# Optimization experiments

Measured on AMD Instinct MI355X. Metric: run time of the kernel, lower is better.

The kernel has to match this reference:

```python
import jax, jax.numpy as jnp
import numpy as np

N_NODES = 100000
N_EDGES = 1600000
D_FEAT = 64
NUM_HEADS = 4
HEAD_CH = 16
ALPHA = 0.2  # leaky_relu negative slope (Keras default)


def setup_inputs() -> dict:
    key = jax.random.key(0)
    ks = jax.random.split(key, 8)
    hc = NUM_HEADS * HEAD_CH
    scale = 1.0 / np.sqrt(D_FEAT)
    return {
        'node_features': jax.random.normal(ks[0], (N_NODES, D_FEAT), jnp.float32),
        'Wq': jax.random.normal(ks[1], (D_FEAT, hc), jnp.float32) * scale,
        'bq': jnp.zeros((hc,), jnp.float32),
        'Wv': jax.random.normal(ks[2], (D_FEAT, hc), jnp.float32) * scale,
        'bv': jnp.zeros((hc,), jnp.float32),
        'attn_kernel': jax.random.normal(ks[3], (HEAD_CH, NUM_HEADS), jnp.float32) / np.sqrt(HEAD_CH),
        'edge_source': jax.random.randint(ks[4], (N_EDGES,), 0, N_NODES, jnp.int32),
        'edge_target': jax.random.randint(ks[5], (N_EDGES,), 0, N_NODES, jnp.int32),
    }


def _gatv2(node_features, Wq, bq, Wv, bv, attn_kernel, edge_source, edge_target):
    # Dense transforms on nodes (small GEMMs), then reshape to heads.
    query = (node_features @ Wq + bq).reshape(N_NODES, NUM_HEADS, HEAD_CH)
    value = (node_features @ Wv + bv).reshape(N_NODES, NUM_HEADS, HEAD_CH)
    # Gather onto edges: receiver query, sender value.
    q_e = query[edge_target]           # [E, H, C]
    v_e = value[edge_source]           # [E, H, C]
    feat = jax.nn.leaky_relu(q_e + v_e, ALPHA)
    # EinsumDense '...ik,ki->...i' with kernel [C, H]
    logits = jnp.einsum('ehc,ch->eh', feat, attn_kernel)  # [E, H]
    # Segment softmax over receiver neighborhoods.
    seg_max = jax.ops.segment_max(logits, edge_target, num_segments=N_NODES)
    seg_max = jnp.where(jnp.isfinite(seg_max), seg_max, 0.0)
    exp = jnp.exp(logits - seg_max[edge_target])           # [E, H]
    denom = jax.ops.segment_sum(exp, edge_target, num_segments=N_NODES)
    denom = jnp.where(denom > 0, denom, 1.0)
    coef = exp / denom[edge_target]                        # [E, H]
    # Weighted scatter-sum of values to receivers.
    pooled = jax.ops.segment_sum(coef[:, :, None] * v_e, edge_target,
                                 num_segments=N_NODES)     # [N, H, C]
    out = pooled.reshape(N_NODES, NUM_HEADS * HEAD_CH)
    # NOTE: source code sets final activation to attention_activation (leaky_relu).
    return jax.nn.leaky_relu(out, ALPHA)


def reference(node_features, Wq, bq, Wv, bv, attn_kernel, edge_source, edge_target):
    return _gatv2(node_features, Wq, bq, Wv, bv, attn_kernel, edge_source, edge_target)
```

## Files before the change

kernel.cpp:

```cpp
#include <hip/hip_runtime.h>

#define NN 100000
#define NE 1600000
#define ALPHA 0.2f

#define BSH   9
#define NPBK  512
#define NBUCK ((NN + NPBK - 1) / NPBK)
#define NPB   256
#define CHUNK ((NE + NPB - 1) / NPB)

#define MTILES (NN / 16)
#define TBLKS  ((MTILES + 3) / 4)

typedef __attribute__((ext_vector_type(8))) short  short8;
typedef __attribute__((ext_vector_type(4))) float  f32x4;

__device__ __forceinline__ unsigned short f2bf(float f) {
    unsigned int u = __builtin_bit_cast(unsigned int, f);
    u += 0x7FFFu + ((u >> 16) & 1u);
    return (unsigned short)(u >> 16);
}
__device__ __forceinline__ float bf2fs(unsigned short u) {
    return __builtin_bit_cast(float, (unsigned int)u << 16);
}
__device__ __forceinline__ float bflo(unsigned int u) {
    return __builtin_bit_cast(float, u << 16);
}
__device__ __forceinline__ float bfhi(unsigned int u) {
    return __builtin_bit_cast(float, u & 0xFFFF0000u);
}

template<int CTRL>
__device__ __forceinline__ float dpp_add(float x) {
    int y = __builtin_amdgcn_update_dpp(0, __builtin_bit_cast(int, x),
                                        CTRL, 0xF, 0xF, true);
    return x + __builtin_bit_cast(float, y);
}

__device__ __forceinline__ int block_excl_scan_256(int val, int* lds4) {
    const int lane = threadIdx.x & 63;
    const int wid  = threadIdx.x >> 6;
    int incl = val;
    #pragma unroll
    for (int off = 1; off < 64; off <<= 1) {
        int t = __shfl_up(incl, off);
        if (lane >= off) incl += t;
    }
    if (lane == 63) lds4[wid] = incl;
    __syncthreads();
    int wbase = 0;
    #pragma unroll
    for (int w = 0; w < 4; w++) if (w < wid) wbase += lds4[w];
    __syncthreads();
    return wbase + incl - val;
}

__device__ __forceinline__ int block_excl_scan_512(int val, int* lds8) {
    const int lane = threadIdx.x & 63;
    const int wid  = threadIdx.x >> 6;
    int incl = val;
    #pragma unroll
    for (int off = 1; off < 64; off <<= 1) {
        int t = __shfl_up(incl, off);
        if (lane >= off) incl += t;
    }
    if (lane == 63) lds8[wid] = incl;
    __syncthreads();
    int wbase = 0;
    #pragma unroll
    for (int w = 0; w < 8; w++) if (w < wid) wbase += lds8[w];
    __syncthreads();
    return wbase + incl - val;
}

__global__ __launch_bounds__(256) void fused_tc_kernel(
    const float* __restrict__ nf, const float* __restrict__ Wq, const float* __restrict__ bq,
    const float* __restrict__ Wv, const float* __restrict__ bv,
    unsigned short* __restrict__ qbf, unsigned short* __restrict__ vbf,
    const int* __restrict__ etgt, int* __restrict__ hist)
{
    __shared__ short8 sB[2][2][8][64];
    __shared__ float  sbias[128];
    __shared__ int    h[NBUCK];
    const int tid = threadIdx.x;

    if (blockIdx.x < NPB) {
        const int blk = blockIdx.x;
        for (int i = tid; i < NBUCK; i += 256) h[i] = 0;
        __syncthreads();
        const int e0 = blk * CHUNK;
        const int e1 = min(e0 + CHUNK, NE);
        for (int e = e0 + tid; e < e1; e += 256)
            atomicAdd(&h[etgt[e] >> BSH], 1);
        __syncthreads();
        for (int i = tid; i < NBUCK; i += 256)
            hist[blk * NBUCK + i] = h[i];
        return;
    }

    if (tid < 64)       sbias[tid] = bq[tid];
    else if (tid < 128) sbias[tid] = bv[tid - 64];

    for (int slot = tid; slot < 2 * 8 * 64; slot += 256) {
        const int lane  = slot & 63;
        const int ntile = (slot >> 6) & 7;
        const int kstep = slot >> 9;
        const int j     = ntile * 16 + (lane & 15);
        const int kbase = kstep * 32 + (lane >> 4) * 8;
        const float* W  = (j < 64) ? Wq : Wv;
        const int jj    = j & 63;
        short8 hi, lo;
        #pragma unroll
        for (int r = 0; r < 8; r++) {
            float w = W[(kbase + r) * 64 + jj];
            unsigned short hh = f2bf(w);
            lo[r] = (short)f2bf(w - bf2fs(hh));
            hi[r] = (short)hh;
        }
        sB[0][kstep][ntile][lane] = hi;
        sB[1][kstep][ntile][lane] = lo;
    }
    __syncthreads();

    const int lane  = tid & 63;
    const int wv_   = tid >> 6;
    const int row16 = lane & 15;
    const int kg    = lane >> 4;
    const int tb    = blockIdx.x - NPB;

    for (int wt = tb * 4 + wv_; wt < MTILES; wt += TBLKS * 4) {
        const int row = wt * 16 + row16;

        short8 ah[2];
        #pragma unroll
        for (int s = 0; s < 2; s++) {
            const float* ap = nf + (size_t)row * 64 + s * 32 + kg * 8;
            #pragma unroll
            for (int r = 0; r < 8; r++)
                ah[s][r] = (short)f2bf(ap[r]);
        }

        #pragma unroll
        for (int nt = 0; nt < 8; nt++) {
            f32x4 acc = {0.f, 0.f, 0.f, 0.f};
            #pragma unroll
            for (int s = 0; s < 2; s++) {
                acc = __builtin_amdgcn_mfma_f32_16x16x32_bf16(ah[s], sB[0][s][nt][lane], acc, 0, 0, 0);
                acc = __builtin_amdgcn_mfma_f32_16x16x32_bf16(ah[s], sB[1][s][nt][lane], acc, 0, 0, 0);
            }
            const int col = nt * 16 + (lane & 15);
            const float b = sbias[col];
            unsigned short* outp = (col < 64) ? qbf : vbf;
            const int jj    = col & 63;
            const int rbase = wt * 16 + (lane >> 4) * 4;
            #pragma unroll
            for (int r = 0; r < 4; r++)
                outp[(size_t)(rbase + r) * 64 + jj] = f2bf(acc[r] + b);
        }
    }
}

__global__ __launch_bounds__(256) void colbase_kernel(
    const int* __restrict__ hist,
    int* __restrict__ bbase, int* __restrict__ colbase, int* __restrict__ offs)
{
    __shared__ int lds4[4];
    __shared__ int sb[256];
    const int bk = blockIdx.x;
    const int t  = threadIdx.x;

    int csum = 0;
    if (t < NBUCK) {
        #pragma unroll 8
        for (int b = 0; b < NPB; b++) csum += hist[b * NBUCK + t];
    }
    int gex = block_excl_scan_256(csum, lds4);
    sb[t] = gex;
    if (t == bk) bbase[bk] = gex;
    if (bk == 0 && t == NBUCK - 1) { bbase[NBUCK] = gex + csum; offs[NN] = NE; }
    __syncthreads();
    const int myBase = sb[bk];
    __syncthreads();

    int val = hist[t * NBUCK + bk];
    int ex  = block_excl_scan_256(val, lds4);
    colbase[t * NBUCK + bk] = myBase + ex;
}

__global__ __launch_bounds__(256) void partition_kernel(
    const int* __restrict__ esrc, const int* __restrict__ etgt,
    const int* __restrict__ colbase, unsigned int* __restrict__ packed)
{
    __shared__ int cur[NBUCK];
    const int blk = blockIdx.x;
    for (int i = threadIdx.x; i < NBUCK; i += 256)
        cur[i] = colbase[blk * NBUCK + i];
    __syncthreads();
    const int e0 = blk * CHUNK;
    const int e1 = min(e0 + CHUNK, NE);
    for (int e = e0 + threadIdx.x; e < e1; e += 256) {
        int t = etgt[e], s = esrc[e];
        int bk = t >> BSH;
        int pos = atomicAdd(&cur[bk], 1);
        packed[pos] = (unsigned)s | ((unsigned)(t & (NPBK - 1)) << 17);
    }
}

__global__ __launch_bounds__(512) void bucket_csr_kernel(
    const unsigned int* __restrict__ packed, const int* __restrict__ bbase,
    int* __restrict__ offs, int* __restrict__ ssrc)
{
    __shared__ int cnt[NPBK];
    __shared__ int lds8[8];
    const int bk  = blockIdx.x;
    const int tid = threadIdx.x;
    const int s0 = bbase[bk], s1 = bbase[bk + 1];
    cnt[tid] = 0;
    __syncthreads();
    for (int e = s0 + tid; e < s1; e += 512)
        atomicAdd(&cnt[packed[e] >> 17], 1);
    __syncthreads();
    int a  = cnt[tid];
    int ex = block_excl_scan_512(a, lds8);
    const int node = (bk << BSH) + tid;
    const int g = s0 + ex;
    if (node < NN) offs[node] = g;
    __syncthreads();
    cnt[tid] = g;
    __syncthreads();
    for (int e = s0 + tid; e < s1; e += 512) {
        unsigned p = packed[e];
        int pos = atomicAdd(&cnt[p >> 17], 1);
        ssrc[pos] = (int)(p & 0x1FFFFu);
    }
}

__device__ __forceinline__ uint4 ldraw16(const unsigned short* __restrict__ vb,
                                         int src, int s8) {
    return *(const uint4*)((const char*)vb + ((size_t)src << 7) + s8 * 16);
}

__global__ __launch_bounds__(256) void gather_kernel(
    const unsigned short* __restrict__ qb, const unsigned short* __restrict__ vb,
    const float* __restrict__ ak,
    const int* __restrict__ offs, const int* __restrict__ ssrc,
    float* __restrict__ out)
{
    const int node = (blockIdx.x * 256 + threadIdx.x) >> 6;
    const int lane = threadIdx.x & 63;
    if (node >= NN) return;
    const int eslot = lane >> 3;
    const int s8    = lane & 7;
    const int h     = s8 >> 1;

    const int start = offs[node];
    const int end   = offs[node + 1];

    if (start >= end) {
        if (lane < 8) {
            float4 z{0.f, 0.f, 0.f, 0.f};
            *(float4*)(out + (size_t)node * 64 + s8 * 8)     = z;
            *(float4*)(out + (size_t)node * 64 + s8 * 8 + 4) = z;
        }
        return;
    }
    const int end1 = end - 1;

    const float c6 = 0.6f * 1.44269504088896f;
    const float c4 = 0.4f * 1.44269504088896f;
    float a6[8], a4[8];
    #pragma unroll
    for (int j = 0; j < 8; j++) {
        float k = ak[((s8 & 1) * 8 + j) * 4 + h];
        a6[j] = c6 * k;  a4[j] = c4 * k;
    }

    const uint4 qraw = *(const uint4*)((const char*)qb + ((size_t)node << 7) + s8 * 16);
    float q[8];
    q[0] = bflo(qraw.x); q[1] = bfhi(qraw.x);
    q[2] = bflo(qraw.y); q[3] = bfhi(qraw.y);
    q[4] = bflo(qraw.z); q[5] = bfhi(qraw.z);
    q[6] = bflo(qraw.w); q[7] = bfhi(qraw.w);

    int i0 = ssrc[min(start +     eslot, end1)];
    int i1 = ssrc[min(start + 8 + eslot, end1)];
    uint4 rr0 = ldraw16(vb, i0, s8);
    uint4 rr1 = ldraw16(vb, i1, s8);
    int mi0 = ssrc[min(start + 16 + eslot, end1)];
    int mi1 = ssrc[min(start + 24 + eslot, end1)];

    float acc[8] = {0.f, 0.f, 0.f, 0.f, 0.f, 0.f, 0.f, 0.f};
    float ws = 0.f;

    for (int p = start; p < end; p += 16) {
        {
            float v[8];
            v[0] = bflo(rr0.x); v[1] = bfhi(rr0.x);
            v[2] = bflo(rr0.y); v[3] = bfhi(rr0.y);
            v[4] = bflo(rr0.z); v[5] = bfhi(rr0.z);
            v[6] = bflo(rr0.w); v[7] = bfhi(rr0.w);
            rr0 = ldraw16(vb, mi0, s8);
            mi0 = ssrc[min(p + 32 + eslot, end1)];
            float x = 0.f;
            #pragma unroll
            for (int j = 0; j < 8; j++) {
                float f = q[j] + v[j];
                x = fmaf(f, a6[j], x);
                x = fmaf(fabsf(f), a4[j], x);
            }
            x = dpp_add<0xB1>(x);
            float w = (p + eslot < end) ? __builtin_amdgcn_exp2f(x) : 0.f;
            ws += w;
            #pragma unroll
            for (int j = 0; j < 8; j++) acc[j] = fmaf(w, v[j], acc[j]);
        }
        {
            float v[8];
            v[0] = bflo(rr1.x); v[1] = bfhi(rr1.x);
            v[2] = bflo(rr1.y); v[3] = bfhi(rr1.y);
            v[4] = bflo(rr1.z); v[5] = bfhi(rr1.z);
            v[6] = bflo(rr1.w); v[7] = bfhi(rr1.w);
            rr1 = ldraw16(vb, mi1, s8);
            mi1 = ssrc[min(p + 40 + eslot, end1)];
            float x = 0.f;
            #pragma unroll
            for (int j = 0; j < 8; j++) {
                float f = q[j] + v[j];
                x = fmaf(f, a6[j], x);
                x = fmaf(fabsf(f), a4[j], x);
            }
            x = dpp_add<0xB1>(x);
            float w = (p + 8 + eslot < end) ? __builtin_amdgcn_exp2f(x) : 0.f;
            ws += w;
            #pragma unroll
            for (int j = 0; j < 8; j++) acc[j] = fmaf(w, v[j], acc[j]);
        }
    }

    #pragma unroll
    for (int m = 8; m <= 32; m <<= 1) {
        #pragma unroll
        for (int j = 0; j < 8; j++) acc[j] += __shfl_xor(acc[j], m);
        ws += __shfl_xor(ws, m);
    }

    if (lane < 8) {
        float inv = (ws > 0.f) ? __frcp_rn(ws) : 1.0f;
        float r[8];
        #pragma unroll
        for (int j = 0; j < 8; j++) {
            float t = acc[j] * inv;
            r[j] = fmaxf(t, ALPHA * t);
        }
        *(float4*)(out + (size_t)node * 64 + s8 * 8)     = float4{r[0], r[1], r[2], r[3]};
        *(float4*)(out + (size_t)node * 64 + s8 * 8 + 4) = float4{r[4], r[5], r[6], r[7]};
    }
}

extern "C" void kernel_launch(void* const* d_in, const int* in_sizes, int n_in,
                              void* d_out, int out_size, void* d_ws, size_t ws_size,
                              hipStream_t stream) {
    const float* nf   = (const float*)d_in[0];
    const float* Wq   = (const float*)d_in[1];
    const float* bq   = (const float*)d_in[2];
    const float* Wv   = (const float*)d_in[3];
    const float* bv   = (const float*)d_in[4];
    const float* ak   = (const float*)d_in[5];
    const int*   esrc = (const int*)d_in[6];
    const int*   etgt = (const int*)d_in[7];
    float* out = (float*)d_out;

    unsigned short* qbf     = (unsigned short*)d_ws;
    unsigned short* vbf     = qbf + (size_t)NN * 64;
    int*            offs    = (int*)(vbf + (size_t)NN * 64);
    int*            ssrc    = offs + (NN + 1);
    unsigned int*   packed  = (unsigned int*)(ssrc + NE);
    int*            hist    = (int*)(packed + NE);
    int*            colbase = hist + NPB * NBUCK;
    int*            bbase   = colbase + NPB * NBUCK;

    fused_tc_kernel<<<NPB + TBLKS, 256, 0, stream>>>(nf, Wq, bq, Wv, bv, qbf, vbf,
                                                     etgt, hist);
    colbase_kernel<<<NBUCK, 256, 0, stream>>>(hist, bbase, colbase, offs);
    partition_kernel<<<NPB, 256, 0, stream>>>(esrc, etgt, colbase, packed);
    bucket_csr_kernel<<<NBUCK, 512, 0, stream>>>(packed, bbase, offs, ssrc);
    gather_kernel<<<(NN * 64 + 255) / 256, 256, 0, stream>>>(qbf, vbf, ak, offs, ssrc, out);
}
```

Before: 113.1 us.

## Spread node transform tiles across all CSR-build kernels to fill idle CUs

The dense Q/V transform is no longer done in one kernel alongside the histogram. Its tiles are split into four fixed ranges, and each range is appended as extra blocks to the histogram, colbase, partition and bucket-CSR kernels. The aim is to overlap the MFMA GEMM work with the latency-bound sort stages, which underuse the GPU. In exchange, every transform block repeats the weight split/prep into shared memory, and the hardcoded tile ranges must cover all tiles exactly.

```diff
diff --git a/kernel.cpp b/kernel.cpp
--- a/kernel.cpp
+++ b/kernel.cpp
@@ -11,7 +11,15 @@
 #define CHUNK ((NE + NPB - 1) / NPB)
 
 #define MTILES (NN / 16)
-#define TBLKS  ((MTILES + 3) / 4)
+
+#define TB1 0
+#define N1  290
+#define TB2 1160
+#define N2  145
+#define TB3 1740
+#define N3  638
+#define TB4 4292
+#define N4  245
 
 typedef __attribute__((ext_vector_type(8))) short  short8;
 typedef __attribute__((ext_vector_type(4))) float  f32x4;
@@ -74,35 +82,14 @@
     return wbase + incl - val;
 }
 
-__global__ __launch_bounds__(256) void fused_tc_kernel(
-    const float* __restrict__ nf, const float* __restrict__ Wq, const float* __restrict__ bq,
+__device__ __forceinline__ void transform_prep(
+    const float* __restrict__ Wq, const float* __restrict__ bq,
     const float* __restrict__ Wv, const float* __restrict__ bv,
-    unsigned short* __restrict__ qbf, unsigned short* __restrict__ vbf,
-    const int* __restrict__ etgt, int* __restrict__ hist)
-{
-    __shared__ short8 sB[2][2][8][64];
-    __shared__ float  sbias[128];
-    __shared__ int    h[NBUCK];
-    const int tid = threadIdx.x;
-
-    if (blockIdx.x < NPB) {
-        const int blk = blockIdx.x;
-        for (int i = tid; i < NBUCK; i += 256) h[i] = 0;
-        __syncthreads();
-        const int e0 = blk * CHUNK;
-        const int e1 = min(e0 + CHUNK, NE);
-        for (int e = e0 + tid; e < e1; e += 256)
-            atomicAdd(&h[etgt[e] >> BSH], 1);
-        __syncthreads();
-        for (int i = tid; i < NBUCK; i += 256)
-            hist[blk * NBUCK + i] = h[i];
-        return;
-    }
-
+    short8 (*sB)[2][8][64], float* sbias, int tid, int nthr)
+{
     if (tid < 64)       sbias[tid] = bq[tid];
     else if (tid < 128) sbias[tid] = bv[tid - 64];
-
-    for (int slot = tid; slot < 2 * 8 * 64; slot += 256) {
+    for (int slot = tid; slot < 2 * 8 * 64; slot += nthr) {
         const int lane  = slot & 63;
         const int ntile = (slot >> 6) & 7;
         const int kstep = slot >> 9;
@@ -121,119 +108,187 @@
         sB[0][kstep][ntile][lane] = hi;
         sB[1][kstep][ntile][lane] = lo;
     }
-    __syncthreads();
-
-    const int lane  = tid & 63;
-    const int wv_   = tid >> 6;
-    const int row16 = lane & 15;
-    const int kg    = lane >> 4;
-    const int tb    = blockIdx.x - NPB;
-
-    for (int wt = tb * 4 + wv_; wt < MTILES; wt += TBLKS * 4) {
-        const int row = wt * 16 + row16;
-
-        short8 ah[2];
+}
+
+__device__ __forceinline__ void transform_tile(
+    const float* __restrict__ nf,
+    unsigned short* __restrict__ qbf, unsigned short* __restrict__ vbf,
+    short8 (*sB)[2][8][64], const float* sbias, int wt, int lane)
+{
+    const int row = wt * 16 + (lane & 15);
+    short8 ah[2];
+    #pragma unroll
+    for (int s = 0; s < 2; s++) {
+        const float* ap = nf + (size_t)row * 64 + s * 32 + (lane >> 4) * 8;
+        #pragma unroll
+        for (int r = 0; r < 8; r++)
+            ah[s][r] = (short)f2bf(ap[r]);
+    }
+    #pragma unroll
+    for (int nt = 0; nt < 8; nt++) {
+        f32x4 acc = {0.f, 0.f, 0.f, 0.f};
         #pragma unroll
         for (int s = 0; s < 2; s++) {
-            const float* ap = nf + (size_t)row * 64 + s * 32 + kg * 8;
-            #pragma unroll
-            for (int r = 0; r < 8; r++)
-                ah[s][r] = (short)f2bf(ap[r]);
-        }
-
-        #pragma unroll
-        for (int nt = 0; nt < 8; nt++) {
-            f32x4 acc = {0.f, 0.f, 0.f, 0.f};
-            #pragma unroll
-            for (int s = 0; s < 2; s++) {
-                acc = __builtin_amdgcn_mfma_f32_16x16x32_bf16(ah[s], sB[0][s][nt][lane], acc, 0, 0, 0);
-                acc = __builtin_amdgcn_mfma_f32_16x16x32_bf16(ah[s], sB[1][s][nt][lane], acc, 0, 0, 0);
-            }
-            const int col = nt * 16 + (lane & 15);
-            const float b = sbias[col];
-            unsigned short* outp = (col < 64) ? qbf : vbf;
-            const int jj    = col & 63;
-            const int rbase = wt * 16 + (lane >> 4) * 4;
-            #pragma unroll
-            for (int r = 0; r < 4; r++)
-                outp[(size_t)(rbase + r) * 64 + jj] = f2bf(acc[r] + b);
-        }
-    }
-}
-
-__global__ __launch_bounds__(256) void colbase_kernel(
+            acc = __builtin_amdgcn_mfma_f32_16x16x32_bf16(ah[s], sB[0][s][nt][lane], acc, 0, 0, 0);
+            acc = __builtin_amdgcn_mfma_f32_16x16x32_bf16(ah[s], sB[1][s][nt][lane], acc, 0, 0, 0);
+        }
+        const int col = nt * 16 + (lane & 15);
+        const float b = sbias[col];
+        unsigned short* outp = (col < 64) ? qbf : vbf;
+        const int jj    = col & 63;
+        const int rbase = wt * 16 + (lane >> 4) * 4;
+        #pragma unroll
+        for (int r = 0; r < 4; r++)
+            outp[(size_t)(rbase + r) * 64 + jj] = f2bf(acc[r] + b);
+    }
+}
+
+__global__ __launch_bounds__(256) void k1_hist_tf(
+    const float* __restrict__ nf, const float* __restrict__ Wq, const float* __restrict__ bq,
+    const float* __restrict__ Wv, const float* __restrict__ bv,
+    unsigned short* __restrict__ qbf, unsigned short* __restrict__ vbf,
+    const int* __restrict__ etgt, int* __restrict__ hist)
+{
+    __shared__ short8 sB[2][2][8][64];
+    __shared__ float  sbias[128];
+    __shared__ int    h[NBUCK];
+    const int tid = threadIdx.x;
+
+    if (blockIdx.x < NPB) {
+        const int blk = blockIdx.x;
+        for (int i = tid; i < NBUCK; i += 256) h[i] = 0;
+        __syncthreads();
+        const int e0 = blk * CHUNK;
+        const int e1 = min(e0 + CHUNK, NE);
+        for (int e = e0 + tid; e < e1; e += 256)
+            atomicAdd(&h[etgt[e] >> BSH], 1);
+        __syncthreads();
+        for (int i = tid; i < NBUCK; i += 256)
+            hist[blk * NBUCK + i] = h[i];
+        return;
+    }
+
+    transform_prep(Wq, bq, Wv, bv, sB, sbias, tid, 256);
+    __syncthreads();
+    const int wt = TB1 + ((int)blockIdx.x - NPB) * 4 + (tid >> 6);
+    if (wt < MTILES) transform_tile(nf, qbf, vbf, sB, sbias, wt, tid & 63);
+}
+
+__global__ __launch_bounds__(256) void k2_colbase_tf(
+    const float* __restrict__ nf, const float* __restrict__ Wq, const float* __restrict__ bq,
+    const float* __restrict__ Wv, const float* __restrict__ bv,
+    unsigned short* __restrict__ qbf, unsigned short* __restrict__ vbf,
     const int* __restrict__ hist,
     int* __restrict__ bbase, int* __restrict__ colbase, int* __restrict__ offs)
 {
+    __shared__ short8 sB[2][2][8][64];
+    __shared__ float  sbias[128];
     __shared__ int lds4[4];
     __shared__ int sb[256];
-    const int bk = blockIdx.x;
-    const int t  = threadIdx.x;
-
-    int csum = 0;
-    if (t < NBUCK) {
-        #pragma unroll 8
-        for (int b = 0; b < NPB; b++) csum += hist[b * NBUCK + t];
-    }
-    int gex = block_excl_scan_256(csum, lds4);
-    sb[t] = gex;
-    if (t == bk) bbase[bk] = gex;
-    if (bk == 0 && t == NBUCK - 1) { bbase[NBUCK] = gex + csum; offs[NN] = NE; }
-    __syncthreads();
-    const int myBase = sb[bk];
-    __syncthreads();
-
-    int val = hist[t * NBUCK + bk];
-    int ex  = block_excl_scan_256(val, lds4);
-    colbase[t * NBUCK + bk] = myBase + ex;
-}
-
-__global__ __launch_bounds__(256) void partition_kernel(
+    const int t = threadIdx.x;
+
+    if (blockIdx.x < NBUCK) {
+        const int bk = blockIdx.x;
+        int csum = 0;
+        if (t < NBUCK) {
+            #pragma unroll 8
+            for (int b = 0; b < NPB; b++) csum += hist[b * NBUCK + t];
+        }
+        int gex = block_excl_scan_256(csum, lds4);
+        sb[t] = gex;
+        if (t == bk) bbase[bk] = gex;
+        if (bk == 0 && t == NBUCK - 1) { bbase[NBUCK] = gex + csum; offs[NN] = NE; }
+        __syncthreads();
+        const int myBase = sb[bk];
+        __syncthreads();
+
+        int val = hist[t * NBUCK + bk];
+        int ex  = block_excl_scan_256(val, lds4);
+        colbase[t * NBUCK + bk] = myBase + ex;
+        return;
+    }
+
+    transform_prep(Wq, bq, Wv, bv, sB, sbias, t, 256);
+    __syncthreads();
+    const int wt = TB2 + ((int)blockIdx.x - NBUCK) * 4 + (t >> 6);
+    if (wt < MTILES) transform_tile(nf, qbf, vbf, sB, sbias, wt, t & 63);
+}
+
+__global__ __launch_bounds__(256) void k3_partition_tf(
+    const float* __restrict__ nf, const float* __restrict__ Wq, const float* __restrict__ bq,
+    const float* __restrict__ Wv, const float* __restrict__ bv,
+    unsigned short* __restrict__ qbf, unsigned short* __restrict__ vbf,
     const int* __restrict__ esrc, const int* __restrict__ etgt,
     const int* __restrict__ colbase, unsigned int* __restrict__ packed)
 {
+    __shared__ short8 sB[2][2][8][64];
+    __shared__ float  sbias[128];
     __shared__ int cur[NBUCK];
-    const int blk = blockIdx.x;
-    for (int i = threadIdx.x; i < NBUCK; i += 256)
-        cur[i] = colbase[blk * NBUCK + i];
-    __syncthreads();
-    const int e0 = blk * CHUNK;
-    const int e1 = min(e0 + CHUNK, NE);
-    for (int e = e0 + threadIdx.x; e < e1; e += 256) {
-        int t = etgt[e], s = esrc[e];
-        int bk = t >> BSH;
-        int pos = atomicAdd(&cur[bk], 1);
-        packed[pos] = (unsigned)s | ((unsigned)(t & (NPBK - 1)) << 17);
-    }
-}
-
-__global__ __launch_bounds__(512) void bucket_csr_kernel(
+    const int tid = threadIdx.x;
+
+    if (blockIdx.x < NPB) {
+        const int blk = blockIdx.x;
+        for (int i = tid; i < NBUCK; i += 256)
+            cur[i] = colbase[blk * NBUCK + i];
+        __syncthreads();
+        const int e0 = blk * CHUNK;
+        const int e1 = min(e0 + CHUNK, NE);
+        for (int e = e0 + tid; e < e1; e += 256) {
+            int t = etgt[e], s = esrc[e];
+            int bk = t >> BSH;
+            int pos = atomicAdd(&cur[bk], 1);
+            packed[pos] = (unsigned)s | ((unsigned)(t & (NPBK - 1)) << 17);
+        }
+        return;
+    }
+
+    transform_prep(Wq, bq, Wv, bv, sB, sbias, tid, 256);
+    __syncthreads();
+    const int wt = TB3 + ((int)blockIdx.x - NPB) * 4 + (tid >> 6);
+    if (wt < MTILES) transform_tile(nf, qbf, vbf, sB, sbias, wt, tid & 63);
+}
+
+__global__ __launch_bounds__(512) void k4_csr_tf(
+    const float* __restrict__ nf, const float* __restrict__ Wq, const float* __restrict__ bq,
+    const float* __restrict__ Wv, const float* __restrict__ bv,
+    unsigned short* __restrict__ qbf, unsigned short* __restrict__ vbf,
     const unsigned int* __restrict__ packed, const int* __restrict__ bbase,
     int* __restrict__ offs, int* __restrict__ ssrc)
 {
+    __shared__ short8 sB[2][2][8][64];
+    __shared__ float  sbias[128];
     __shared__ int cnt[NPBK];
     __shared__ int lds8[8];
-    const int bk  = blockIdx.x;
     const int tid = threadIdx.x;
-    const int s0 = bbase[bk], s1 = bbase[bk + 1];
-    cnt[tid] = 0;
-    __syncthreads();
-    for (int e = s0 + tid; e < s1; e += 512)
-        atomicAdd(&cnt[packed[e] >> 17], 1);
-    __syncthreads();
-    int a  = cnt[tid];
-    int ex = block_excl_scan_512(a, lds8);
-    const int node = (bk << BSH) + tid;
-    const int g = s0 + ex;
-    if (node < NN) offs[node] = g;
-    __syncthreads();
-    cnt[tid] = g;
-    __syncthreads();
-    for (int e = s0 + tid; e < s1; e += 512) {
-        unsigned p = packed[e];
-        int pos = atomicAdd(&cnt[p >> 17], 1);
-        ssrc[pos] = (int)(p & 0x1FFFFu);
-    }
+
+    if (blockIdx.x < NBUCK) {
+        const int bk = blockIdx.x;
+        const int s0 = bbase[bk], s1 = bbase[bk + 1];
+        cnt[tid] = 0;
+        __syncthreads();
+        for (int e = s0 + tid; e < s1; e += 512)
+            atomicAdd(&cnt[packed[e] >> 17], 1);
+        __syncthreads();
+        int a  = cnt[tid];
+        int ex = block_excl_scan_512(a, lds8);
+        const int node = (bk << BSH) + tid;
+        const int g = s0 + ex;
+        if (node < NN) offs[node] = g;
+        __syncthreads();
+        cnt[tid] = g;
+        __syncthreads();
+        for (int e = s0 + tid; e < s1; e += 512) {
+            unsigned p = packed[e];
+            int pos = atomicAdd(&cnt[p >> 17], 1);
+            ssrc[pos] = (int)(p & 0x1FFFFu);
+        }
+        return;
+    }
+
+    transform_prep(Wq, bq, Wv, bv, sB, sbias, tid, 512);
+    __syncthreads();
+    const int wt = TB4 + ((int)blockIdx.x - NBUCK) * 8 + (tid >> 6);
+    if (wt < MTILES) transform_tile(nf, qbf, vbf, sB, sbias, wt, tid & 63);
 }
 
 __device__ __forceinline__ uint4 ldraw16(const unsigned short* __restrict__ vb,
@@ -380,10 +435,12 @@
     int*            colbase = hist + NPB * NBUCK;
     int*            bbase   = colbase + NPB * NBUCK;
 
-    fused_tc_kernel<<<NPB + TBLKS, 256, 0, stream>>>(nf, Wq, bq, Wv, bv, qbf, vbf,
-                                                     etgt, hist);
-    colbase_kernel<<<NBUCK, 256, 0, stream>>>(hist, bbase, colbase, offs);
-    partition_kernel<<<NPB, 256, 0, stream>>>(esrc, etgt, colbase, packed);
-    bucket_csr_kernel<<<NBUCK, 512, 0, stream>>>(packed, bbase, offs, ssrc);
+    k1_hist_tf<<<NPB + N1, 256, 0, stream>>>(nf, Wq, bq, Wv, bv, qbf, vbf, etgt, hist);
+    k2_colbase_tf<<<NBUCK + N2, 256, 0, stream>>>(nf, Wq, bq, Wv, bv, qbf, vbf,
+                                                  hist, bbase, colbase, offs);
+    k3_partition_tf<<<NPB + N3, 256, 0, stream>>>(nf, Wq, bq, Wv, bv, qbf, vbf,
+                                                  esrc, etgt, colbase, packed);
+    k4_csr_tf<<<NBUCK + N4, 512, 0, stream>>>(nf, Wq, bq, Wv, bv, qbf, vbf,
+                                              packed, bbase, offs, ssrc);
     gather_kernel<<<(NN * 64 + 255) / 256, 256, 0, stream>>>(qbf, vbf, ak, offs, ssrc, out);
 }
```

Result: faster. 105.3 us (-6.9%).

## Merge histogram, partition and CSR into two kernels with split dense transform

Applied to the files above, without the earlier changes.

The separate colbase scan and partition pass are replaced by a one-pass partition that reserves per-bucket space with global atomics into fixed-capacity MAXB bucket slabs. The CSR build then scans bucket totals inside each block. The dense Q/V transform is split across both kernels so that it overlaps with the partition and CSR work, which cuts the number of launches and the global scan passes. In exchange it adds a memset, leaves edge order within a bucket nondeterministic, and assumes no bucket ever exceeds MAXB edges.

```diff
diff --git a/kernel.cpp b/kernel.cpp
--- a/kernel.cpp
+++ b/kernel.cpp
@@ -9,9 +9,12 @@
 #define NBUCK ((NN + NPBK - 1) / NPBK)
 #define NPB   256
 #define CHUNK ((NE + NPB - 1) / NPB)
+#define MAXB  16384
 
 #define MTILES (NN / 16)
-#define TBLKS  ((MTILES + 3) / 4)
+#define TSPLIT 3440
+#define NA     (TSPLIT / 4)
+#define NB     (((MTILES - TSPLIT) + 7) / 8)
 
 typedef __attribute__((ext_vector_type(8))) short  short8;
 typedef __attribute__((ext_vector_type(4))) float  f32x4;
@@ -38,24 +41,6 @@
     return x + __builtin_bit_cast(float, y);
 }
 
-__device__ __forceinline__ int block_excl_scan_256(int val, int* lds4) {
-    const int lane = threadIdx.x & 63;
-    const int wid  = threadIdx.x >> 6;
-    int incl = val;
-    #pragma unroll
-    for (int off = 1; off < 64; off <<= 1) {
-        int t = __shfl_up(incl, off);
-        if (lane >= off) incl += t;
-    }
-    if (lane == 63) lds4[wid] = incl;
-    __syncthreads();
-    int wbase = 0;
-    #pragma unroll
-    for (int w = 0; w < 4; w++) if (w < wid) wbase += lds4[w];
-    __syncthreads();
-    return wbase + incl - val;
-}
-
 __device__ __forceinline__ int block_excl_scan_512(int val, int* lds8) {
     const int lane = threadIdx.x & 63;
     const int wid  = threadIdx.x >> 6;
@@ -74,35 +59,14 @@
     return wbase + incl - val;
 }
 
-__global__ __launch_bounds__(256) void fused_tc_kernel(
-    const float* __restrict__ nf, const float* __restrict__ Wq, const float* __restrict__ bq,
+__device__ __forceinline__ void transform_prep(
+    const float* __restrict__ Wq, const float* __restrict__ bq,
     const float* __restrict__ Wv, const float* __restrict__ bv,
-    unsigned short* __restrict__ qbf, unsigned short* __restrict__ vbf,
-    const int* __restrict__ etgt, int* __restrict__ hist)
-{
-    __shared__ short8 sB[2][2][8][64];
-    __shared__ float  sbias[128];
-    __shared__ int    h[NBUCK];
-    const int tid = threadIdx.x;
-
-    if (blockIdx.x < NPB) {
-        const int blk = blockIdx.x;
-        for (int i = tid; i < NBUCK; i += 256) h[i] = 0;
-        __syncthreads();
-        const int e0 = blk * CHUNK;
-        const int e1 = min(e0 + CHUNK, NE);
-        for (int e = e0 + tid; e < e1; e += 256)
-            atomicAdd(&h[etgt[e] >> BSH], 1);
-        __syncthreads();
-        for (int i = tid; i < NBUCK; i += 256)
-            hist[blk * NBUCK + i] = h[i];
-        return;
-    }
-
+    short8 (*sB)[2][8][64], float* sbias, int tid, int nthr)
+{
     if (tid < 64)       sbias[tid] = bq[tid];
     else if (tid < 128) sbias[tid] = bv[tid - 64];
-
-    for (int slot = tid; slot < 2 * 8 * 64; slot += 256) {
+    for (int slot = tid; slot < 2 * 8 * 64; slot += nthr) {
         const int lane  = slot & 63;
         const int ntile = (slot >> 6) & 7;
         const int kstep = slot >> 9;
@@ -121,119 +85,132 @@
         sB[0][kstep][ntile][lane] = hi;
         sB[1][kstep][ntile][lane] = lo;
     }
+}
+
+__device__ __forceinline__ void transform_tile(
+    const float* __restrict__ nf,
+    unsigned short* __restrict__ qbf, unsigned short* __restrict__ vbf,
+    short8 (*sB)[2][8][64], const float* sbias, int wt, int lane)
+{
+    const int row = wt * 16 + (lane & 15);
+    short8 ah[2];
+    #pragma unroll
+    for (int s = 0; s < 2; s++) {
+        const float* ap = nf + (size_t)row * 64 + s * 32 + (lane >> 4) * 8;
+        #pragma unroll
+        for (int r = 0; r < 8; r++)
+            ah[s][r] = (short)f2bf(ap[r]);
+    }
+    #pragma unroll
+    for (int nt = 0; nt < 8; nt++) {
+        f32x4 acc = {0.f, 0.f, 0.f, 0.f};
+        #pragma unroll
+        for (int s = 0; s < 2; s++) {
+            acc = __builtin_amdgcn_mfma_f32_16x16x32_bf16(ah[s], sB[0][s][nt][lane], acc, 0, 0, 0);
+            acc = __builtin_amdgcn_mfma_f32_16x16x32_bf16(ah[s], sB[1][s][nt][lane], acc, 0, 0, 0);
+        }
+        const int col = nt * 16 + (lane & 15);
+        const float b = sbias[col];
+        unsigned short* outp = (col < 64) ? qbf : vbf;
+        const int jj    = col & 63;
+        const int rbase = wt * 16 + (lane >> 4) * 4;
+        #pragma unroll
+        for (int r = 0; r < 4; r++)
+            outp[(size_t)(rbase + r) * 64 + jj] = f2bf(acc[r] + b);
+    }
+}
+
+__global__ __launch_bounds__(256) void kA_partition_tf(
+    const float* __restrict__ nf, const float* __restrict__ Wq, const float* __restrict__ bq,
+    const float* __restrict__ Wv, const float* __restrict__ bv,
+    unsigned short* __restrict__ qbf, unsigned short* __restrict__ vbf,
+    const int* __restrict__ esrc, const int* __restrict__ etgt,
+    int* __restrict__ gcur, unsigned int* __restrict__ packed)
+{
+    __shared__ short8 sB[2][2][8][64];
+    __shared__ float  sbias[128];
+    __shared__ int    h[NBUCK];
+    const int tid = threadIdx.x;
+    const int bid = blockIdx.x;
+
+    if (bid < NPB) {
+        for (int i = tid; i < NBUCK; i += 256) h[i] = 0;
+        __syncthreads();
+        const int e0 = bid * CHUNK;
+        const int e1 = min(e0 + CHUNK, NE);
+        for (int e = e0 + tid; e < e1; e += 256)
+            atomicAdd(&h[etgt[e] >> BSH], 1);
+        __syncthreads();
+        for (int i = tid; i < NBUCK; i += 256) {
+            int c = h[i];
+            h[i] = c ? atomicAdd(&gcur[i], c) : 0;
+        }
+        __syncthreads();
+        for (int e = e0 + tid; e < e1; e += 256) {
+            int t = etgt[e], s = esrc[e];
+            int bk = t >> BSH;
+            int o = atomicAdd(&h[bk], 1);
+            packed[(size_t)bk * MAXB + o] = (unsigned)s | ((unsigned)(t & (NPBK - 1)) << 17);
+        }
+        return;
+    }
+
+    transform_prep(Wq, bq, Wv, bv, sB, sbias, tid, 256);
     __syncthreads();
-
-    const int lane  = tid & 63;
-    const int wv_   = tid >> 6;
-    const int row16 = lane & 15;
-    const int kg    = lane >> 4;
-    const int tb    = blockIdx.x - NPB;
-
-    for (int wt = tb * 4 + wv_; wt < MTILES; wt += TBLKS * 4) {
-        const int row = wt * 16 + row16;
-
-        short8 ah[2];
-        #pragma unroll
-        for (int s = 0; s < 2; s++) {
-            const float* ap = nf + (size_t)row * 64 + s * 32 + kg * 8;
-            #pragma unroll
-            for (int r = 0; r < 8; r++)
-                ah[s][r] = (short)f2bf(ap[r]);
-        }
-
-        #pragma unroll
-        for (int nt = 0; nt < 8; nt++) {
-            f32x4 acc = {0.f, 0.f, 0.f, 0.f};
-            #pragma unroll
-            for (int s = 0; s < 2; s++) {
-                acc = __builtin_amdgcn_mfma_f32_16x16x32_bf16(ah[s], sB[0][s][nt][lane], acc, 0, 0, 0);
-                acc = __builtin_amdgcn_mfma_f32_16x16x32_bf16(ah[s], sB[1][s][nt][lane], acc, 0, 0, 0);
-            }
-            const int col = nt * 16 + (lane & 15);
-            const float b = sbias[col];
-            unsigned short* outp = (col < 64) ? qbf : vbf;
-            const int jj    = col & 63;
-            const int rbase = wt * 16 + (lane >> 4) * 4;
-            #pragma unroll
-            for (int r = 0; r < 4; r++)
-                outp[(size_t)(rbase + r) * 64 + jj] = f2bf(acc[r] + b);
-        }
-    }
-}
-
-__global__ __launch_bounds__(256) void colbase_kernel(
-    const int* __restrict__ hist,
-    int* __restrict__ bbase, int* __restrict__ colbase, int* __restrict__ offs)
-{
-    __shared__ int lds4[4];
-    __shared__ int sb[256];
-    const int bk = blockIdx.x;
-    const int t  = threadIdx.x;
-
-    int csum = 0;
-    if (t < NBUCK) {
-        #pragma unroll 8
-        for (int b = 0; b < NPB; b++) csum += hist[b * NBUCK + t];
-    }
-    int gex = block_excl_scan_256(csum, lds4);
-    sb[t] = gex;
-    if (t == bk) bbase[bk] = gex;
-    if (bk == 0 && t == NBUCK - 1) { bbase[NBUCK] = gex + csum; offs[NN] = NE; }
+    const int wt = (bid - NPB) * 4 + (tid >> 6);
+    if (wt < TSPLIT) transform_tile(nf, qbf, vbf, sB, sbias, wt, tid & 63);
+}
+
+__global__ __launch_bounds__(512) void kB_csr_tf(
+    const float* __restrict__ nf, const float* __restrict__ Wq, const float* __restrict__ bq,
+    const float* __restrict__ Wv, const float* __restrict__ bv,
+    unsigned short* __restrict__ qbf, unsigned short* __restrict__ vbf,
+    const unsigned int* __restrict__ packed, const int* __restrict__ gcur,
+    int* __restrict__ offs, int* __restrict__ ssrc)
+{
+    __shared__ short8 sB[2][2][8][64];
+    __shared__ float  sbias[128];
+    __shared__ int    cnt[NPBK];
+    __shared__ int    lds8[8];
+    __shared__ int    sS0, sSZ;
+    const int tid = threadIdx.x;
+    const int bid = blockIdx.x;
+
+    if (bid < NBUCK) {
+        int val = (tid < NBUCK) ? gcur[tid] : 0;
+        int ex  = block_excl_scan_512(val, lds8);
+        if (tid == bid) { sS0 = ex; sSZ = val; }
+        if (bid == 0 && tid == 0) offs[NN] = NE;
+        __syncthreads();
+        const int s0 = sS0;
+        const int sz = sSZ;
+        const unsigned int* mypack = packed + (size_t)bid * MAXB;
+
+        cnt[tid] = 0;
+        __syncthreads();
+        for (int e = tid; e < sz; e += 512)
+            atomicAdd(&cnt[mypack[e] >> 17], 1);
+        __syncthreads();
+        int a  = cnt[tid];
+        int ex2 = block_excl_scan_512(a, lds8);
+        const int node = (bid << BSH) + tid;
+        const int g = s0 + ex2;
+        if (node < NN) offs[node] = g;
+        __syncthreads();
+        cnt[tid] = g;
+        __syncthreads();
+        for (int e = tid; e < sz; e += 512) {
+            unsigned p = mypack[e];
+            int pos = atomicAdd(&cnt[p >> 17], 1);
+            ssrc[pos] = (int)(p & 0x1FFFFu);
+        }
+        return;
+    }
+
+    transform_prep(Wq, bq, Wv, bv, sB, sbias, tid, 512);
     __syncthreads();
-    const int myBase = sb[bk];
-    __syncthreads();
-
-    int val = hist[t * NBUCK + bk];
-    int ex  = block_excl_scan_256(val, lds4);
-    colbase[t * NBUCK + bk] = myBase + ex;
-}
-
-__global__ __launch_bounds__(256) void partition_kernel(
-    const int* __restrict__ esrc, const int* __restrict__ etgt,
-    const int* __restrict__ colbase, unsigned int* __restrict__ packed)
-{
-    __shared__ int cur[NBUCK];
-    const int blk = blockIdx.x;
-    for (int i = threadIdx.x; i < NBUCK; i += 256)
-        cur[i] = colbase[blk * NBUCK + i];
-    __syncthreads();
-    const int e0 = blk * CHUNK;
-    const int e1 = min(e0 + CHUNK, NE);
-    for (int e = e0 + threadIdx.x; e < e1; e += 256) {
-        int t = etgt[e], s = esrc[e];
-        int bk = t >> BSH;
-        int pos = atomicAdd(&cur[bk], 1);
-        packed[pos] = (unsigned)s | ((unsigned)(t & (NPBK - 1)) << 17);
-    }
-}
-
-__global__ __launch_bounds__(512) void bucket_csr_kernel(
-    const unsigned int* __restrict__ packed, const int* __restrict__ bbase,
-    int* __restrict__ offs, int* __restrict__ ssrc)
-{
-    __shared__ int cnt[NPBK];
-    __shared__ int lds8[8];
-    const int bk  = blockIdx.x;
-    const int tid = threadIdx.x;
-    const int s0 = bbase[bk], s1 = bbase[bk + 1];
-    cnt[tid] = 0;
-    __syncthreads();
-    for (int e = s0 + tid; e < s1; e += 512)
-        atomicAdd(&cnt[packed[e] >> 17], 1);
-    __syncthreads();
-    int a  = cnt[tid];
-    int ex = block_excl_scan_512(a, lds8);
-    const int node = (bk << BSH) + tid;
-    const int g = s0 + ex;
-    if (node < NN) offs[node] = g;
-    __syncthreads();
-    cnt[tid] = g;
-    __syncthreads();
-    for (int e = s0 + tid; e < s1; e += 512) {
-        unsigned p = packed[e];
-        int pos = atomicAdd(&cnt[p >> 17], 1);
-        ssrc[pos] = (int)(p & 0x1FFFFu);
-    }
+    const int wt = TSPLIT + (bid - NBUCK) * 8 + (tid >> 6);
+    if (wt < MTILES) transform_tile(nf, qbf, vbf, sB, sbias, wt, tid & 63);
 }
 
 __device__ __forceinline__ uint4 ldraw16(const unsigned short* __restrict__ vb,
@@ -371,19 +348,18 @@
     const int*   etgt = (const int*)d_in[7];
     float* out = (float*)d_out;
 
-    unsigned short* qbf     = (unsigned short*)d_ws;
-    unsigned short* vbf     = qbf + (size_t)NN * 64;
-    int*            offs    = (int*)(vbf + (size_t)NN * 64);
-    int*            ssrc    = offs + (NN + 1);
-    unsigned int*   packed  = (unsigned int*)(ssrc + NE);
-    int*            hist    = (int*)(packed + NE);
-    int*            colbase = hist + NPB * NBUCK;
-    int*            bbase   = colbase + NPB * NBUCK;
-
-    fused_tc_kernel<<<NPB + TBLKS, 256, 0, stream>>>(nf, Wq, bq, Wv, bv, qbf, vbf,
-                                                     etgt, hist);
-    colbase_kernel<<<NBUCK, 256, 0, stream>>>(hist, bbase, colbase, offs);
-    partition_kernel<<<NPB, 256, 0, stream>>>(esrc, etgt, colbase, packed);
-    bucket_csr_kernel<<<NBUCK, 512, 0, stream>>>(packed, bbase, offs, ssrc);
+    unsigned short* qbf    = (unsigned short*)d_ws;
+    unsigned short* vbf    = qbf + (size_t)NN * 64;
+    int*            offs   = (int*)(vbf + (size_t)NN * 64);
+    int*            ssrc   = offs + (NN + 1);
+    unsigned int*   packed = (unsigned int*)(ssrc + NE);
+    int*            gcur   = (int*)(packed + (size_t)NBUCK * MAXB);
+
+    hipMemsetAsync(gcur, 0, NBUCK * sizeof(int), stream);
+
+    kA_partition_tf<<<NPB + NA, 256, 0, stream>>>(nf, Wq, bq, Wv, bv, qbf, vbf,
+                                                  esrc, etgt, gcur, packed);
+    kB_csr_tf<<<NBUCK + NB, 512, 0, stream>>>(nf, Wq, bq, Wv, bv, qbf, vbf,
+                                              packed, gcur, offs, ssrc);
     gather_kernel<<<(NN * 64 + 255) / 256, 256, 0, stream>>>(qbf, vbf, ak, offs, ssrc, out);
 }
```

After: 106.0 us. 6.3% less time.
